# Kernel optimization log

Measured on AMD Instinct MI355X. Metric: run time of the kernel, lower is better.

Reference implementation:

```python
import jax, jax.numpy as jnp
import numpy as np
import math

B, S, F, R = 16, 2048, 512, 4
EPS = 1e-5

def setup_inputs() -> dict:
    key = jax.random.key(0)
    ks = jax.random.split(key, 8)
    s = 1.0 / math.sqrt(S)
    return {
        "x": jax.random.normal(ks[0], (B, S, F), dtype=jnp.float32),
        "Wq": jax.random.uniform(ks[1], (R, S), jnp.float32, -s, s),
        "bq": jnp.zeros((R,), jnp.float32),
        "Wk": jax.random.uniform(ks[2], (R, S), jnp.float32, -s, s),
        "bk": jnp.zeros((R,), jnp.float32),
        "Wv": jax.random.uniform(ks[3], (S, S), jnp.float32, -s, s),
        "bv": jnp.zeros((S,), jnp.float32),
        "ln_w": jnp.ones((S, F), jnp.float32),
        "ln_b": jnp.zeros((S, F), jnp.float32),
        "alpha": jnp.asarray(0.1, jnp.float32),
        "beta": jnp.asarray(0.1, jnp.float32),
    }

def reference(x, Wq, bq, Wk, bk, Wv, bv, ln_w, ln_b, alpha, beta):
    # LayerNorm over last two dims [S, F]
    mu = jnp.mean(x, axis=(1, 2), keepdims=True)
    var = jnp.mean(jnp.square(x - mu), axis=(1, 2), keepdims=True)
    x_norm = (x - mu) * jax.lax.rsqrt(var + EPS) * ln_w + ln_b
    x_t = jnp.swapaxes(x_norm, 1, 2)  # [B, F, S]
    Q = jnp.einsum('bfs,rs->bfr', x_t, Wq) + bq  # [B, F, R]
    K = jnp.einsum('bfs,rs->bfr', x_t, Wk) + bk  # [B, F, R]
    A = jnp.einsum('bfr,bgr->bfg', Q, K) / math.sqrt(R)  # [B, F, F]
    A = jax.nn.softmax(A, axis=-1)
    V = jnp.einsum('bfs,ts->bft', x_t, Wv) + bv  # [B, F, S]
    out = jnp.einsum('bfg,bgs->bfs', A, V)  # [B, F, S]
    # dropout in eval mode = identity
    out = x_t + alpha * out + V + beta * V
    return jnp.swapaxes(out, 1, 2)  # [B, S, F]
```

## Files before the change

### kernel.cpp

```cpp
#include <hip/hip_runtime.h>
#include <hip/hip_bf16.h>

#define NB 16
#define SS 2048
#define FF 512

typedef __bf16 bf16_t;
typedef __bf16 bf16x8 __attribute__((ext_vector_type(8)));
typedef __bf16 bf16x4 __attribute__((ext_vector_type(4)));
typedef float  f32x4  __attribute__((ext_vector_type(4)));

__global__ __launch_bounds__(256) void stats_kernel(const float* __restrict__ x,
                                                    float* __restrict__ partials) {
    const int b = blockIdx.y;
    const float* xb = x + ((size_t)b << 20) + (size_t)blockIdx.x * 16384;
    float s = 0.0f, ss = 0.0f;
#pragma unroll
    for (int i = 0; i < 16; ++i) {
        const float4 v = *(const float4*)&xb[(threadIdx.x + i * 256) * 4];
        s  += v.x + v.y + v.z + v.w;
        ss += v.x * v.x + v.y * v.y + v.z * v.z + v.w * v.w;
    }
#pragma unroll
    for (int off = 32; off > 0; off >>= 1) {
        s  += __shfl_down(s, off);
        ss += __shfl_down(ss, off);
    }
    __shared__ float ps[4], pss[4];
    const int w = threadIdx.x >> 6, lane = threadIdx.x & 63;
    if (lane == 0) { ps[w] = s; pss[w] = ss; }
    __syncthreads();
    if (threadIdx.x == 0) {
        partials[b * 64 + blockIdx.x]        = ps[0] + ps[1] + ps[2] + ps[3];
        partials[1024 + b * 64 + blockIdx.x] = pss[0] + pss[1] + pss[2] + pss[3];
    }
}

__global__ __launch_bounds__(256) void finalize_stats(const float* __restrict__ partials,
                                                      float* __restrict__ musig) {
    const int tid = threadIdx.x;
    const int b = tid >> 4, i = tid & 15;
    float s = 0.f, ss = 0.f;
#pragma unroll
    for (int j = 0; j < 4; ++j) {
        s  += partials[b * 64 + i * 4 + j];
        ss += partials[1024 + b * 64 + i * 4 + j];
    }
#pragma unroll
    for (int off = 8; off > 0; off >>= 1) {
        s  += __shfl_xor(s, off);
        ss += __shfl_xor(ss, off);
    }
    if (i == 0) {
        const float inv_n = 1.0f / 1048576.0f;
        const float mu  = s * inv_n;
        const float var = ss * inv_n - mu * mu;
        musig[b]      = mu;
        musig[16 + b] = rsqrtf(var + 1e-5f);
    }
}

__global__ __launch_bounds__(256) void ynorm_kernel(const float* __restrict__ x,
                                                    const float* __restrict__ lw,
                                                    const float* __restrict__ lb,
                                                    const float* __restrict__ musig,
                                                    bf16_t* __restrict__ Y,
                                                    bf16_t* __restrict__ Xn) {
    __shared__ bf16_t t[32][36];
    const int b = blockIdx.z;
    const int f0 = blockIdx.x * 32, s0 = blockIdx.y * 32;
    const float mu = musig[b], rs = musig[16 + b];
    const int tid = threadIdx.x;
    {
        const int s_loc = tid >> 3, c4 = (tid & 7) * 4;
        const size_t idx = (size_t)(s0 + s_loc) * FF + f0 + c4;
        const float4 xv = *(const float4*)&x[((size_t)b << 20) + idx];
        const float4 wv = *(const float4*)&lw[idx];
        const float4 bv = *(const float4*)&lb[idx];
        bf16x4 o;
        o[0] = (bf16_t)((xv.x - mu) * rs * wv.x + bv.x);
        o[1] = (bf16_t)((xv.y - mu) * rs * wv.y + bv.y);
        o[2] = (bf16_t)((xv.z - mu) * rs * wv.z + bv.z);
        o[3] = (bf16_t)((xv.w - mu) * rs * wv.w + bv.w);
        t[s_loc][c4 + 0] = o[0];
        t[s_loc][c4 + 1] = o[1];
        t[s_loc][c4 + 2] = o[2];
        t[s_loc][c4 + 3] = o[3];
        if (Xn) *(bf16x4*)&Xn[((size_t)b << 20) + idx] = o;
    }
    __syncthreads();
    {
        const int f_loc = tid >> 3, s4 = (tid & 7) * 4;
        bf16x4 o;
        o[0] = t[s4 + 0][f_loc];
        o[1] = t[s4 + 1][f_loc];
        o[2] = t[s4 + 2][f_loc];
        o[3] = t[s4 + 3][f_loc];
        *(bf16x4*)&Y[((size_t)b << 20) + (size_t)(f0 + f_loc) * SS + s0 + s4] = o;
    }
}

__global__ __launch_bounds__(256) void cast_wv(const float* __restrict__ Wv,
                                               bf16_t* __restrict__ Wvb) {
    const size_t i = ((size_t)blockIdx.x * 256 + threadIdx.x) * 4;
    const float4 v = *(const float4*)&Wv[i];
    bf16x4 o;
    o[0] = (bf16_t)v.x; o[1] = (bf16_t)v.y; o[2] = (bf16_t)v.z; o[3] = (bf16_t)v.w;
    *(bf16x4*)&Wvb[i] = o;
}

__global__ __launch_bounds__(256) void qk_kernel(const bf16_t* __restrict__ Y,
                                                 const float* __restrict__ Wq,
                                                 const float* __restrict__ bq,
                                                 const float* __restrict__ Wk,
                                                 const float* __restrict__ bk,
                                                 float* __restrict__ Qo,
                                                 float* __restrict__ Ko) {
    const int w = threadIdx.x >> 6, lane = threadIdx.x & 63;
    const int row0 = blockIdx.x * 16 + w * 4;
    const bf16_t* y0 = Y + (size_t)row0 * SS;
    float qa[4][4] = {}, ka[4][4] = {};
#pragma unroll
    for (int c = 0; c < 4; ++c) {
        const int s = c * 512 + lane * 8;
        float yf[4][8];
#pragma unroll
        for (int rr = 0; rr < 4; ++rr) {
            const bf16x8 yv = *(const bf16x8*)&y0[(size_t)rr * SS + s];
#pragma unroll
            for (int j = 0; j < 8; ++j) yf[rr][j] = (float)yv[j];
        }
#pragma unroll
        for (int r = 0; r < 4; ++r) {
            const float4 a0 = *(const float4*)&Wq[r * SS + s];
            const float4 a1 = *(const float4*)&Wq[r * SS + s + 4];
            const float4 c0 = *(const float4*)&Wk[r * SS + s];
            const float4 c1 = *(const float4*)&Wk[r * SS + s + 4];
#pragma unroll
            for (int rr = 0; rr < 4; ++rr) {
                qa[rr][r] += yf[rr][0]*a0.x + yf[rr][1]*a0.y + yf[rr][2]*a0.z + yf[rr][3]*a0.w
                           + yf[rr][4]*a1.x + yf[rr][5]*a1.y + yf[rr][6]*a1.z + yf[rr][7]*a1.w;
                ka[rr][r] += yf[rr][0]*c0.x + yf[rr][1]*c0.y + yf[rr][2]*c0.z + yf[rr][3]*c0.w
                           + yf[rr][4]*c1.x + yf[rr][5]*c1.y + yf[rr][6]*c1.z + yf[rr][7]*c1.w;
            }
        }
    }
#pragma unroll
    for (int off = 32; off > 0; off >>= 1) {
#pragma unroll
        for (int rr = 0; rr < 4; ++rr)
#pragma unroll
            for (int r = 0; r < 4; ++r) {
                qa[rr][r] += __shfl_down(qa[rr][r], off);
                ka[rr][r] += __shfl_down(ka[rr][r], off);
            }
    }
    if (lane == 0) {
#pragma unroll
        for (int rr = 0; rr < 4; ++rr)
#pragma unroll
            for (int r = 0; r < 4; ++r) {
                Qo[(size_t)(row0 + rr) * 4 + r] = qa[rr][r] + bq[r];
                Ko[(size_t)(row0 + rr) * 4 + r] = ka[rr][r] + bk[r];
            }
    }
}

__global__ __launch_bounds__(256) void softmax_kernel(const float* __restrict__ Qo,
                                                      const float* __restrict__ Ko,
                                                      bf16_t* __restrict__ Aout) {
    const int w = threadIdx.x >> 6, lane = threadIdx.x & 63;
    const int row = blockIdx.x * 4 + w;
    const int b = row >> 9;
    const float4 q = *(const float4*)&Qo[(size_t)row * 4];
    const float* kb = Ko + (size_t)b * FF * 4;
    float sc[8];
#pragma unroll
    for (int j = 0; j < 8; ++j) {
        const float4 kv = *(const float4*)&kb[(lane * 8 + j) * 4];
        sc[j] = (q.x*kv.x + q.y*kv.y + q.z*kv.z + q.w*kv.w) * 0.5f;
    }
    float mx = sc[0];
#pragma unroll
    for (int j = 1; j < 8; ++j) mx = fmaxf(mx, sc[j]);
#pragma unroll
    for (int off = 32; off > 0; off >>= 1) mx = fmaxf(mx, __shfl_xor(mx, off));
    float sum = 0.f;
#pragma unroll
    for (int j = 0; j < 8; ++j) { sc[j] = __expf(sc[j] - mx); sum += sc[j]; }
#pragma unroll
    for (int off = 32; off > 0; off >>= 1) sum += __shfl_xor(sum, off);
    const float inv = 1.0f / sum;
    bf16x8 o;
#pragma unroll
    for (int j = 0; j < 8; ++j) o[j] = (bf16_t)(sc[j] * inv);
    *(bf16x8*)&Aout[(size_t)row * FF + lane * 8] = o;
}

template<int EPI>
__device__ __forceinline__ void gemm_impl(
        const bf16_t* __restrict__ Abase, long long strideA, int lda,
        const bf16_t* __restrict__ Bbase, long long strideB, int ldb,
        bf16_t* __restrict__ Cbase, long long strideC, int ldc,
        int NTILES, const float* __restrict__ bias_m,
        const float* __restrict__ xp, const float* __restrict__ lwp,
        const float* __restrict__ lbp, const bf16_t* __restrict__ xnp,
        const float* __restrict__ musig,
        const float* __restrict__ alphap, const float* __restrict__ betap,
        float* __restrict__ outp) {
    __shared__ __align__(16) bf16_t As[2][16384];
    __shared__ __align__(16) bf16_t Bs[2][16384];
    const int tid = threadIdx.x;
    const int w = tid >> 6, lane = tid & 63;

    const int nchunk = gridDim.x >> 3;
    const int wgid = (blockIdx.x & 7) * nchunk + (blockIdx.x >> 3);
    const int bz = wgid >> 4;
    const int rem = wgid & 15;
    const int m0 = (rem & 7) * 256, n0 = (rem >> 3) * 256;

    const bf16_t* A = Abase + (size_t)bz * (size_t)strideA;
    const bf16_t* B = Bbase + (size_t)bz * (size_t)strideB;
    bf16_t* C = Cbase + (size_t)bz * (size_t)strideC;
    const int wm = w >> 2, wn = w & 3;

    const int rr0 = (w * 2 + 0) * 16 + (lane >> 2);
    const int rr1 = (w * 2 + 1) * 16 + (lane >> 2);
    const int sw0 = ((lane & 3) ^ ((rr0 >> 1) & 3)) * 8;
    const int sw1 = ((lane & 3) ^ ((rr1 >> 1) & 3)) * 8;
    const bf16_t* gA0 = A + (size_t)(m0 + rr0) * lda + sw0;
    const bf16_t* gA1 = A + (size_t)(m0 + rr1) * lda + sw1;
    const bf16_t* gB0 = B + (size_t)(n0 + rr0) * ldb + sw0;
    const bf16_t* gB1 = B + (size_t)(n0 + rr1) * ldb + sw1;
    const int d0 = (w * 2 + 0) * 512;
    const int d1 = (w * 2 + 1) * 512;

#define STA(bi, h, ko) do {                                                          \
    __builtin_amdgcn_global_load_lds(                                                \
        (const __attribute__((address_space(1))) unsigned int*)(gA0 + (ko) + (h)*32),\
        (__attribute__((address_space(3))) unsigned int*)&As[bi][(h)*8192 + d0], 16, 0, 0); \
    __builtin_amdgcn_global_load_lds(                                                \
        (const __attribute__((address_space(1))) unsigned int*)(gA1 + (ko) + (h)*32),\
        (__attribute__((address_space(3))) unsigned int*)&As[bi][(h)*8192 + d1], 16, 0, 0); \
} while (0)
#define STB(bi, h, ko) do {                                                          \
    __builtin_amdgcn_global_load_lds(                                                \
        (const __attribute__((address_space(1))) unsigned int*)(gB0 + (ko) + (h)*32),\
        (__attribute__((address_space(3))) unsigned int*)&Bs[bi][(h)*8192 + d0], 16, 0, 0); \
    __builtin_amdgcn_global_load_lds(                                                \
        (const __attribute__((address_space(1))) unsigned int*)(gB1 + (ko) + (h)*32),\
        (__attribute__((address_space(3))) unsigned int*)&Bs[bi][(h)*8192 + d1], 16, 0, 0); \
} while (0)

    const int cs = lane >> 4;
    int offA[2][8], offB[2][4];
#pragma unroll
    for (int kk = 0; kk < 2; ++kk) {
#pragma unroll
        for (int mt = 0; mt < 8; ++mt) {
            const int r = wm * 128 + mt * 16 + (lane & 15);
            offA[kk][mt] = kk * 8192 + r * 32 + ((cs ^ ((r >> 1) & 3)) << 3);
        }
#pragma unroll
        for (int nt = 0; nt < 4; ++nt) {
            const int r = wn * 64 + nt * 16 + (lane & 15);
            offB[kk][nt] = kk * 8192 + r * 32 + ((cs ^ ((r >> 1) & 3)) << 3);
        }
    }

#define RD_A(dst, base, kk, mh) do { _Pragma("unroll")                        \
    for (int i = 0; i < 4; ++i) dst[i] = *(const bf16x8*)&(base)[offA[kk][(mh)*4 + i]]; } while (0)
#define RD_B(dst, base, kk) do { _Pragma("unroll")                            \
    for (int i = 0; i < 4; ++i) dst[i] = *(const bf16x8*)&(base)[offB[kk][i]]; } while (0)
#define MFMA16X(af, bfr, mh) do { _Pragma("unroll")                           \
    for (int i = 0; i < 4; ++i) { _Pragma("unroll")                           \
        for (int nt = 0; nt < 4; ++nt)                                        \
            acc[(mh)*4 + i][nt] = __builtin_amdgcn_mfma_f32_16x16x32_bf16(    \
                af[i], bfr[nt], acc[(mh)*4 + i][nt], 0, 0, 0); } } while (0)
#define VMC(n) asm volatile("s_waitcnt vmcnt(" #n ")" ::: "memory")
#define HBAR  __builtin_amdgcn_s_barrier()
#define LGKM(n) do { asm volatile("s_waitcnt lgkmcnt(" #n ")" ::: "memory");  \
                     __builtin_amdgcn_sched_barrier(0); } while (0)
#define SBAR  __builtin_amdgcn_sched_barrier(0)
#define PRIO1 __builtin_amdgcn_s_setprio(1)
#define PRIO0 __builtin_amdgcn_s_setprio(0)

    f32x4 acc[8][4] = {};
    bf16x8 afA[4], afB[4], bfrA[4], bfrB[4];
    const int mask = NTILES - 1;

    STA(0, 0, 0); STB(0, 0, 0); STA(0, 1, 0); STB(0, 1, 0);
    VMC(4); HBAR;
    RD_A(afA, As[0], 0, 0); RD_B(bfrA, Bs[0], 0);

    for (int t = 0; t < NTILES; ++t) {
        const int cur = t & 1, oth = cur ^ 1;
        const int ko = ((t + 1) & mask) * 64;
        const bf16_t* as  = As[cur];
        const bf16_t* bs  = Bs[cur];
        const bf16_t* asn = As[oth];
        const bf16_t* bsn = Bs[oth];
        RD_A(afB, as, 0, 1); SBAR;
        STA(oth, 0, ko); SBAR;
        LGKM(4);
        PRIO1; MFMA16X(afA, bfrA, 0); PRIO0; SBAR;
        VMC(2); HBAR;
        RD_A(afA, as, 1, 0); RD_B(bfrB, bs, 1); SBAR;
        STB(oth, 0, ko); SBAR;
        LGKM(8);
        PRIO1; MFMA16X(afB, bfrA, 1); PRIO0; SBAR;
        RD_A(afB, as, 1, 1); SBAR;
        STA(oth, 1, ko); SBAR;
        LGKM(4);
        PRIO1; MFMA16X(afA, bfrB, 0); PRIO0; SBAR;
        VMC(2); HBAR;
        RD_A(afA, asn, 0, 0); RD_B(bfrA, bsn, 0); SBAR;
        STB(oth, 1, ko); SBAR;
        LGKM(8);
        PRIO1; MFMA16X(afB, bfrB, 1); PRIO0; SBAR;
    }
#undef STA
#undef STB
#undef RD_A
#undef RD_B
#undef MFMA16X
#undef VMC
#undef HBAR
#undef LGKM
#undef SBAR
#undef PRIO1
#undef PRIO0

    if constexpr (EPI == 0) {
#pragma unroll
        for (int mt = 0; mt < 8; ++mt) {
#pragma unroll
            for (int r = 0; r < 4; ++r) {
                const int row = m0 + wm * 128 + mt * 16 + ((lane >> 4) << 2) + r;
                const float bm = bias_m ? bias_m[row] : 0.0f;
#pragma unroll
                for (int nt = 0; nt < 4; ++nt) {
                    const int col = n0 + wn * 64 + nt * 16 + (lane & 15);
                    C[(size_t)row * ldc + col] = (bf16_t)(acc[mt][nt][r] + bm);
                }
            }
        }
    } else {
        asm volatile("s_waitcnt vmcnt(0) lgkmcnt(0)" ::: "memory");
        __syncthreads();
        float* lsc0 = (float*)&As[0][0];
        float* lsc1 = (float*)&As[1][0];
        const float alpha = alphap[0];
        const float onepb = 1.0f + betap[0];
        float mu = 0.f, rs = 0.f;
        if constexpr (EPI == 1) { mu = musig[bz]; rs = musig[16 + bz]; }
        const float* xb = (EPI == 1) ? xp + ((size_t)bz << 20) : nullptr;
        const bf16_t* xnb = (EPI == 2) ? xnp + ((size_t)bz << 20) : nullptr;
        float* ob = outp + ((size_t)bz << 20);
        const int lrow = wm * 16 + ((lane >> 4) << 2);
        const int lcol = wn * 64 + (lane & 15);
        const int gr = tid >> 4;
        const int gc = (tid & 15) * 16;
#define SCAT(mt, bank) do { _Pragma("unroll")                                 \
    for (int r = 0; r < 4; ++r) { _Pragma("unroll")                           \
        for (int nt = 0; nt < 4; ++nt)                                        \
            (bank)[(lrow + r) * 256 + lcol + nt * 16] = acc[mt][nt][r]; } } while (0)
        SCAT(0, lsc0);
        __syncthreads();
#pragma unroll
        for (int mt = 0; mt < 8; ++mt) {
            float* bank  = (mt & 1) ? lsc1 : lsc0;
            float* nbank = (mt & 1) ? lsc0 : lsc1;
            const int grow = m0 + (gr >> 4) * 128 + mt * 16 + (gr & 15);
            const size_t idx = (size_t)grow * FF + n0 + gc;
            const bf16x8 vt0 = *(const bf16x8*)&A[(size_t)grow * lda + n0 + gc];
            const bf16x8 vt1 = *(const bf16x8*)&A[(size_t)grow * lda + n0 + gc + 8];
            bf16x8 xn0, xn1;
            float4 xv[4], wv[4], bv4[4];
            if constexpr (EPI == 2) {
                xn0 = *(const bf16x8*)&xnb[idx];
                xn1 = *(const bf16x8*)&xnb[idx + 8];
            } else {
#pragma unroll
                for (int j = 0; j < 4; ++j) {
                    xv[j]  = *(const float4*)&xb[idx + j * 4];
                    wv[j]  = *(const float4*)&lwp[idx + j * 4];
                    bv4[j] = *(const float4*)&lbp[idx + j * 4];
                }
            }
            if (mt < 7) {
                switch (mt + 1) {
                    case 1: SCAT(1, nbank); break;
                    case 2: SCAT(2, nbank); break;
                    case 3: SCAT(3, nbank); break;
                    case 4: SCAT(4, nbank); break;
                    case 5: SCAT(5, nbank); break;
                    case 6: SCAT(6, nbank); break;
                    case 7: SCAT(7, nbank); break;
                }
            }
#pragma unroll
            for (int j = 0; j < 4; ++j) {
                const float4 av = *(const float4*)&bank[gr * 256 + gc + j * 4];
                float4 o;
                if constexpr (EPI == 2) {
                    const int e = (j & 1) * 4;
                    const bf16x8& xs = (j < 2) ? xn0 : xn1;
                    const bf16x8& vs = (j < 2) ? vt0 : vt1;
                    o.x = (float)xs[e + 0] + alpha * av.x + onepb * (float)vs[e + 0];
                    o.y = (float)xs[e + 1] + alpha * av.y + onepb * (float)vs[e + 1];
                    o.z = (float)xs[e + 2] + alpha * av.z + onepb * (float)vs[e + 2];
                    o.w = (float)xs[e + 3] + alpha * av.w + onepb * (float)vs[e + 3];
                } else {
                    const int e = (j & 1) * 4;
                    const bf16x8& vs = (j < 2) ? vt0 : vt1;
                    o.x = (xv[j].x - mu) * rs * wv[j].x + bv4[j].x + alpha * av.x + onepb * (float)vs[e + 0];
                    o.y = (xv[j].y - mu) * rs * wv[j].y + bv4[j].y + alpha * av.y + onepb * (float)vs[e + 1];
                    o.z = (xv[j].z - mu) * rs * wv[j].z + bv4[j].z + alpha * av.z + onepb * (float)vs[e + 2];
                    o.w = (xv[j].w - mu) * rs * wv[j].w + bv4[j].w + alpha * av.w + onepb * (float)vs[e + 3];
                }
                *(float4*)&ob[idx + j * 4] = o;
            }
            __syncthreads();
        }
#undef SCAT
    }
}

__global__ __launch_bounds__(512, 2) void g1_mm(
        const bf16_t* A, long long sA, int lda, const bf16_t* B, long long sB, int ldb,
        bf16_t* C, long long sC, int ldc, int NT, const float* bias_m) {
    gemm_impl<0>(A, sA, lda, B, sB, ldb, C, sC, ldc, NT, bias_m,
                 nullptr, nullptr, nullptr, nullptr, nullptr, nullptr, nullptr, nullptr);
}

__global__ __launch_bounds__(512, 2) void g2_mm_full(
        const bf16_t* A, long long sA, int lda, const bf16_t* B, long long sB, int ldb,
        int NT, const float* xp, const float* lwp, const float* lbp,
        const float* musig, const float* alphap, const float* betap, float* outp) {
    gemm_impl<1>(A, sA, lda, B, sB, ldb, nullptr, 0, FF, NT, nullptr,
                 xp, lwp, lbp, nullptr, musig, alphap, betap, outp);
}

__global__ __launch_bounds__(512, 2) void g2_mm_lite(
        const bf16_t* A, long long sA, int lda, const bf16_t* B, long long sB, int ldb,
        int NT, const bf16_t* xnp,
        const float* musig, const float* alphap, const float* betap, float* outp) {
    gemm_impl<2>(A, sA, lda, B, sB, ldb, nullptr, 0, FF, NT, nullptr,
                 nullptr, nullptr, nullptr, xnp, musig, alphap, betap, outp);
}

extern "C" void kernel_launch(void* const* d_in, const int* in_sizes, int n_in,
                              void* d_out, int out_size, void* d_ws, size_t ws_size,
                              hipStream_t stream) {
    const float* x   = (const float*)d_in[0];
    const float* Wq  = (const float*)d_in[1];
    const float* bq  = (const float*)d_in[2];
    const float* Wk  = (const float*)d_in[3];
    const float* bk  = (const float*)d_in[4];
    const float* Wv  = (const float*)d_in[5];
    const float* bv  = (const float*)d_in[6];
    const float* lw  = (const float*)d_in[7];
    const float* lb  = (const float*)d_in[8];
    const float* alp = (const float*)d_in[9];
    const float* bet = (const float*)d_in[10];
    float* out = (float*)d_out;

    char* ws = (char*)d_ws;
    float*  musig = (float*)(ws + 128);
    float*  Qo    = (float*)(ws + 256);
    float*  Ko    = (float*)(ws + 256 + 131072);
    bf16_t* Wvb   = (bf16_t*)(ws + 262400);
    bf16_t* Asm   = (bf16_t*)(ws + 8651008);
    float*  partials = (float*)(ws + 8651008);
    bf16_t* Vt    = (bf16_t*)(ws + 17039616);
    bf16_t* Y     = (bf16_t*)(ws + 50594048);
    bf16_t* Xn    = (bf16_t*)(ws + 84148480);
    const bool lite = ws_size >= (size_t)117702912;

    stats_kernel<<<dim3(64, 16), 256, 0, stream>>>(x, partials);
    finalize_stats<<<1, 256, 0, stream>>>(partials, musig);
    cast_wv<<<4096, 256, 0, stream>>>(Wv, Wvb);
    ynorm_kernel<<<dim3(16, 64, 16), 256, 0, stream>>>(x, lw, lb, musig, Y,
                                                       lite ? Xn : (bf16_t*)nullptr);
    qk_kernel<<<512, 256, 0, stream>>>(Y, Wq, bq, Wk, bk, Qo, Ko);
    softmax_kernel<<<2048, 256, 0, stream>>>(Qo, Ko, Asm);
    g1_mm<<<256, 512, 0, stream>>>(Wvb, 0, SS, Y, 1 << 20, SS, Vt, 1 << 20, FF, 32, bv);
    if (lite) {
        g2_mm_lite<<<256, 512, 0, stream>>>(Vt, 1 << 20, FF, Asm, FF * FF, FF, 8,
                                            Xn, musig, alp, bet, out);
    } else {
        g2_mm_full<<<256, 512, 0, stream>>>(Vt, 1 << 20, FF, Asm, FF * FF, FF, 8,
                                            x, lw, lb, musig, alp, bet, out);
    }
}
```

Baseline: 175.0 us.

## Replace V-projection GEMM with 128x128-tile kernel using more workgroups

Adds a dedicated g1_mm2 kernel for the V projection. It uses 128x128 output tiles, 256 threads, 4 waves each owning a 64x64 sub-tile, and a simplified two-phase double-buffered K loop. It launches 1024 workgroups instead of 256 with 256x256 tiles, which raises occupancy and spreads work more evenly across CUs. The cost is lower operand reuse per tile, so more global and LDS traffic per FLOP. The old EPI==0 path is removed from the shared gemm template.

```diff
diff --git a/kernel.cpp b/kernel.cpp
--- a/kernel.cpp
+++ b/kernel.cpp
@@ -197,12 +197,134 @@
     *(bf16x8*)&Aout[(size_t)row * FF + lane * 8] = o;
 }
 
+__global__ __launch_bounds__(256, 2) void g1_mm2(
+        const bf16_t* __restrict__ Abase, long long strideA, int lda,
+        const bf16_t* __restrict__ Bbase, long long strideB, int ldb,
+        bf16_t* __restrict__ Cbase, long long strideC, int ldc,
+        int NTILES, const float* __restrict__ bias_m) {
+    __shared__ __align__(16) bf16_t As[2][8192];
+    __shared__ __align__(16) bf16_t Bs[2][8192];
+    const int tid = threadIdx.x;
+    const int w = tid >> 6, lane = tid & 63;
+
+    const int nchunk = gridDim.x >> 3;
+    const int wgid = (blockIdx.x & 7) * nchunk + (blockIdx.x >> 3);
+    const int bz = wgid >> 6;
+    const int rem = wgid & 63;
+    const int m0 = (rem & 15) * 128, n0 = (rem >> 4) * 128;
+
+    const bf16_t* A = Abase + (size_t)bz * (size_t)strideA;
+    const bf16_t* B = Bbase + (size_t)bz * (size_t)strideB;
+    bf16_t* C = Cbase + (size_t)bz * (size_t)strideC;
+    const int wmm = (w >> 1) * 64, wnn = (w & 1) * 64;
+
+    const int rr0 = (w * 2 + 0) * 16 + (lane >> 2);
+    const int rr1 = (w * 2 + 1) * 16 + (lane >> 2);
+    const int sw0 = ((lane & 3) ^ ((rr0 >> 1) & 3)) * 8;
+    const int sw1 = ((lane & 3) ^ ((rr1 >> 1) & 3)) * 8;
+    const bf16_t* gA0 = A + (size_t)(m0 + rr0) * lda + sw0;
+    const bf16_t* gA1 = A + (size_t)(m0 + rr1) * lda + sw1;
+    const bf16_t* gB0 = B + (size_t)(n0 + rr0) * ldb + sw0;
+    const bf16_t* gB1 = B + (size_t)(n0 + rr1) * ldb + sw1;
+    const int d0 = (w * 2 + 0) * 512;
+    const int d1 = (w * 2 + 1) * 512;
+
+#define STA2(bi, h, ko) do {                                                         \
+    __builtin_amdgcn_global_load_lds(                                                \
+        (const __attribute__((address_space(1))) unsigned int*)(gA0 + (ko) + (h)*32),\
+        (__attribute__((address_space(3))) unsigned int*)&As[bi][(h)*4096 + d0], 16, 0, 0); \
+    __builtin_amdgcn_global_load_lds(                                                \
+        (const __attribute__((address_space(1))) unsigned int*)(gA1 + (ko) + (h)*32),\
+        (__attribute__((address_space(3))) unsigned int*)&As[bi][(h)*4096 + d1], 16, 0, 0); \
+} while (0)
+#define STB2(bi, h, ko) do {                                                         \
+    __builtin_amdgcn_global_load_lds(                                                \
+        (const __attribute__((address_space(1))) unsigned int*)(gB0 + (ko) + (h)*32),\
+        (__attribute__((address_space(3))) unsigned int*)&Bs[bi][(h)*4096 + d0], 16, 0, 0); \
+    __builtin_amdgcn_global_load_lds(                                                \
+        (const __attribute__((address_space(1))) unsigned int*)(gB1 + (ko) + (h)*32),\
+        (__attribute__((address_space(3))) unsigned int*)&Bs[bi][(h)*4096 + d1], 16, 0, 0); \
+} while (0)
+
+    const int cs = lane >> 4;
+    int offA[2][4], offB[2][4];
+#pragma unroll
+    for (int kk = 0; kk < 2; ++kk) {
+#pragma unroll
+        for (int i = 0; i < 4; ++i) {
+            const int ra = wmm + i * 16 + (lane & 15);
+            offA[kk][i] = kk * 4096 + ra * 32 + ((cs ^ ((ra >> 1) & 3)) << 3);
+            const int rb = wnn + i * 16 + (lane & 15);
+            offB[kk][i] = kk * 4096 + rb * 32 + ((cs ^ ((rb >> 1) & 3)) << 3);
+        }
+    }
+
+#define VMC2  asm volatile("s_waitcnt vmcnt(2)" ::: "memory")
+#define HBAR  __builtin_amdgcn_s_barrier()
+#define LGKM0 do { asm volatile("s_waitcnt lgkmcnt(0)" ::: "memory");         \
+                   __builtin_amdgcn_sched_barrier(0); } while (0)
+#define SBAR  __builtin_amdgcn_sched_barrier(0)
+
+    f32x4 acc[4][4] = {};
+    bf16x8 af[4], bfr[4];
+    const int mask = NTILES - 1;
+
+    STA2(0, 0, 0); STB2(0, 0, 0); STA2(0, 1, 0); STB2(0, 1, 0);
+
+#define PHASE(kk, stA, stB)                                                   \
+    VMC2; HBAR;                                                               \
+    _Pragma("unroll")                                                         \
+    for (int i = 0; i < 4; ++i) af[i]  = *(const bf16x8*)&as[offA[kk][i]];    \
+    _Pragma("unroll")                                                         \
+    for (int i = 0; i < 4; ++i) bfr[i] = *(const bf16x8*)&bs[offB[kk][i]];    \
+    SBAR;                                                                     \
+    stA; stB; SBAR;                                                           \
+    LGKM0;                                                                    \
+    __builtin_amdgcn_s_setprio(1);                                            \
+    _Pragma("unroll")                                                         \
+    for (int i = 0; i < 4; ++i) { _Pragma("unroll")                           \
+        for (int nt = 0; nt < 4; ++nt)                                        \
+            acc[i][nt] = __builtin_amdgcn_mfma_f32_16x16x32_bf16(             \
+                af[i], bfr[nt], acc[i][nt], 0, 0, 0); }                       \
+    __builtin_amdgcn_s_setprio(0); SBAR;                                      \
+    HBAR;
+
+    for (int t = 0; t < NTILES; ++t) {
+        const int cur = t & 1, oth = cur ^ 1;
+        const int ko = ((t + 1) & mask) * 64;
+        const bf16_t* as = As[cur];
+        const bf16_t* bs = Bs[cur];
+        PHASE(0, STA2(oth, 0, ko), STB2(oth, 0, ko));
+        PHASE(1, STA2(oth, 1, ko), STB2(oth, 1, ko));
+    }
+#undef PHASE
+#undef STA2
+#undef STB2
+#undef VMC2
+#undef HBAR
+#undef LGKM0
+#undef SBAR
+
+#pragma unroll
+    for (int i = 0; i < 4; ++i) {
+#pragma unroll
+        for (int r = 0; r < 4; ++r) {
+            const int row = m0 + wmm + i * 16 + ((lane >> 4) << 2) + r;
+            const float bm = bias_m ? bias_m[row] : 0.0f;
+#pragma unroll
+            for (int nt = 0; nt < 4; ++nt) {
+                const int col = n0 + wnn + nt * 16 + (lane & 15);
+                C[(size_t)row * ldc + col] = (bf16_t)(acc[i][nt][r] + bm);
+            }
+        }
+    }
+}
+
 template<int EPI>
 __device__ __forceinline__ void gemm_impl(
         const bf16_t* __restrict__ Abase, long long strideA, int lda,
         const bf16_t* __restrict__ Bbase, long long strideB, int ldb,
-        bf16_t* __restrict__ Cbase, long long strideC, int ldc,
-        int NTILES, const float* __restrict__ bias_m,
+        int NTILES,
         const float* __restrict__ xp, const float* __restrict__ lwp,
         const float* __restrict__ lbp, const bf16_t* __restrict__ xnp,
         const float* __restrict__ musig,
@@ -221,7 +343,6 @@
 
     const bf16_t* A = Abase + (size_t)bz * (size_t)strideA;
     const bf16_t* B = Bbase + (size_t)bz * (size_t)strideB;
-    bf16_t* C = Cbase + (size_t)bz * (size_t)strideC;
     const int wm = w >> 2, wn = w & 3;
 
     const int rr0 = (w * 2 + 0) * 16 + (lane >> 2);
@@ -331,114 +452,91 @@
 #undef PRIO1
 #undef PRIO0
 
-    if constexpr (EPI == 0) {
-#pragma unroll
-        for (int mt = 0; mt < 8; ++mt) {
-#pragma unroll
-            for (int r = 0; r < 4; ++r) {
-                const int row = m0 + wm * 128 + mt * 16 + ((lane >> 4) << 2) + r;
-                const float bm = bias_m ? bias_m[row] : 0.0f;
-#pragma unroll
-                for (int nt = 0; nt < 4; ++nt) {
-                    const int col = n0 + wn * 64 + nt * 16 + (lane & 15);
-                    C[(size_t)row * ldc + col] = (bf16_t)(acc[mt][nt][r] + bm);
-                }
-            }
-        }
-    } else {
-        asm volatile("s_waitcnt vmcnt(0) lgkmcnt(0)" ::: "memory");
-        __syncthreads();
-        float* lsc0 = (float*)&As[0][0];
-        float* lsc1 = (float*)&As[1][0];
-        const float alpha = alphap[0];
-        const float onepb = 1.0f + betap[0];
-        float mu = 0.f, rs = 0.f;
-        if constexpr (EPI == 1) { mu = musig[bz]; rs = musig[16 + bz]; }
-        const float* xb = (EPI == 1) ? xp + ((size_t)bz << 20) : nullptr;
-        const bf16_t* xnb = (EPI == 2) ? xnp + ((size_t)bz << 20) : nullptr;
-        float* ob = outp + ((size_t)bz << 20);
-        const int lrow = wm * 16 + ((lane >> 4) << 2);
-        const int lcol = wn * 64 + (lane & 15);
-        const int gr = tid >> 4;
-        const int gc = (tid & 15) * 16;
+    asm volatile("s_waitcnt vmcnt(0) lgkmcnt(0)" ::: "memory");
+    __syncthreads();
+    float* lsc0 = (float*)&As[0][0];
+    float* lsc1 = (float*)&As[1][0];
+    const float alpha = alphap[0];
+    const float onepb = 1.0f + betap[0];
+    float mu = 0.f, rs = 0.f;
+    if constexpr (EPI == 1) { mu = musig[bz]; rs = musig[16 + bz]; }
+    const float* xb = (EPI == 1) ? xp + ((size_t)bz << 20) : nullptr;
+    const bf16_t* xnb = (EPI == 2) ? xnp + ((size_t)bz << 20) : nullptr;
+    float* ob = outp + ((size_t)bz << 20);
+    const int lrow = wm * 16 + ((lane >> 4) << 2);
+    const int lcol = wn * 64 + (lane & 15);
+    const int gr = tid >> 4;
+    const int gc = (tid & 15) * 16;
 #define SCAT(mt, bank) do { _Pragma("unroll")                                 \
     for (int r = 0; r < 4; ++r) { _Pragma("unroll")                           \
         for (int nt = 0; nt < 4; ++nt)                                        \
             (bank)[(lrow + r) * 256 + lcol + nt * 16] = acc[mt][nt][r]; } } while (0)
-        SCAT(0, lsc0);
+    SCAT(0, lsc0);
+    __syncthreads();
+#pragma unroll
+    for (int mt = 0; mt < 8; ++mt) {
+        float* bank  = (mt & 1) ? lsc1 : lsc0;
+        float* nbank = (mt & 1) ? lsc0 : lsc1;
+        const int grow = m0 + (gr >> 4) * 128 + mt * 16 + (gr & 15);
+        const size_t idx = (size_t)grow * FF + n0 + gc;
+        const bf16x8 vt0 = *(const bf16x8*)&A[(size_t)grow * lda + n0 + gc];
+        const bf16x8 vt1 = *(const bf16x8*)&A[(size_t)grow * lda + n0 + gc + 8];
+        bf16x8 xn0, xn1;
+        float4 xv[4], wv[4], bv4[4];
+        if constexpr (EPI == 2) {
+            xn0 = *(const bf16x8*)&xnb[idx];
+            xn1 = *(const bf16x8*)&xnb[idx + 8];
+        } else {
+#pragma unroll
+            for (int j = 0; j < 4; ++j) {
+                xv[j]  = *(const float4*)&xb[idx + j * 4];
+                wv[j]  = *(const float4*)&lwp[idx + j * 4];
+                bv4[j] = *(const float4*)&lbp[idx + j * 4];
+            }
+        }
+        if (mt < 7) {
+            switch (mt + 1) {
+                case 1: SCAT(1, nbank); break;
+                case 2: SCAT(2, nbank); break;
+                case 3: SCAT(3, nbank); break;
+                case 4: SCAT(4, nbank); break;
+                case 5: SCAT(5, nbank); break;
+                case 6: SCAT(6, nbank); break;
+                case 7: SCAT(7, nbank); break;
+            }
+        }
+#pragma unroll
+        for (int j = 0; j < 4; ++j) {
+            const float4 av = *(const float4*)&bank[gr * 256 + gc + j * 4];
+            float4 o;
+            if constexpr (EPI == 2) {
+                const int e = (j & 1) * 4;
+                const bf16x8& xs = (j < 2) ? xn0 : xn1;
+                const bf16x8& vs = (j < 2) ? vt0 : vt1;
+                o.x = (float)xs[e + 0] + alpha * av.x + onepb * (float)vs[e + 0];
+                o.y = (float)xs[e + 1] + alpha * av.y + onepb * (float)vs[e + 1];
+                o.z = (float)xs[e + 2] + alpha * av.z + onepb * (float)vs[e + 2];
+                o.w = (float)xs[e + 3] + alpha * av.w + onepb * (float)vs[e + 3];
+            } else {
+                const int e = (j & 1) * 4;
+                const bf16x8& vs = (j < 2) ? vt0 : vt1;
+                o.x = (xv[j].x - mu) * rs * wv[j].x + bv4[j].x + alpha * av.x + onepb * (float)vs[e + 0];
+                o.y = (xv[j].y - mu) * rs * wv[j].y + bv4[j].y + alpha * av.y + onepb * (float)vs[e + 1];
+                o.z = (xv[j].z - mu) * rs * wv[j].z + bv4[j].z + alpha * av.z + onepb * (float)vs[e + 2];
+                o.w = (xv[j].w - mu) * rs * wv[j].w + bv4[j].w + alpha * av.w + onepb * (float)vs[e + 3];
+            }
+            *(float4*)&ob[idx + j * 4] = o;
+        }
         __syncthreads();
-#pragma unroll
-        for (int mt = 0; mt < 8; ++mt) {
-            float* bank  = (mt & 1) ? lsc1 : lsc0;
-            float* nbank = (mt & 1) ? lsc0 : lsc1;
-            const int grow = m0 + (gr >> 4) * 128 + mt * 16 + (gr & 15);
-            const size_t idx = (size_t)grow * FF + n0 + gc;
-            const bf16x8 vt0 = *(const bf16x8*)&A[(size_t)grow * lda + n0 + gc];
-            const bf16x8 vt1 = *(const bf16x8*)&A[(size_t)grow * lda + n0 + gc + 8];
-            bf16x8 xn0, xn1;
-            float4 xv[4], wv[4], bv4[4];
-            if constexpr (EPI == 2) {
-                xn0 = *(const bf16x8*)&xnb[idx];
-                xn1 = *(const bf16x8*)&xnb[idx + 8];
-            } else {
-#pragma unroll
-                for (int j = 0; j < 4; ++j) {
-                    xv[j]  = *(const float4*)&xb[idx + j * 4];
-                    wv[j]  = *(const float4*)&lwp[idx + j * 4];
-                    bv4[j] = *(const float4*)&lbp[idx + j * 4];
-                }
-            }
-            if (mt < 7) {
-                switch (mt + 1) {
-                    case 1: SCAT(1, nbank); break;
-                    case 2: SCAT(2, nbank); break;
-                    case 3: SCAT(3, nbank); break;
-                    case 4: SCAT(4, nbank); break;
-                    case 5: SCAT(5, nbank); break;
-                    case 6: SCAT(6, nbank); break;
-                    case 7: SCAT(7, nbank); break;
-                }
-            }
-#pragma unroll
-            for (int j = 0; j < 4; ++j) {
-                const float4 av = *(const float4*)&bank[gr * 256 + gc + j * 4];
-                float4 o;
-                if constexpr (EPI == 2) {
-                    const int e = (j & 1) * 4;
-                    const bf16x8& xs = (j < 2) ? xn0 : xn1;
-                    const bf16x8& vs = (j < 2) ? vt0 : vt1;
-                    o.x = (float)xs[e + 0] + alpha * av.x + onepb * (float)vs[e + 0];
-                    o.y = (float)xs[e + 1] + alpha * av.y + onepb * (float)vs[e + 1];
-                    o.z = (float)xs[e + 2] + alpha * av.z + onepb * (float)vs[e + 2];
-                    o.w = (float)xs[e + 3] + alpha * av.w + onepb * (float)vs[e + 3];
-                } else {
-                    const int e = (j & 1) * 4;
-                    const bf16x8& vs = (j < 2) ? vt0 : vt1;
-                    o.x = (xv[j].x - mu) * rs * wv[j].x + bv4[j].x + alpha * av.x + onepb * (float)vs[e + 0];
-                    o.y = (xv[j].y - mu) * rs * wv[j].y + bv4[j].y + alpha * av.y + onepb * (float)vs[e + 1];
-                    o.z = (xv[j].z - mu) * rs * wv[j].z + bv4[j].z + alpha * av.z + onepb * (float)vs[e + 2];
-                    o.w = (xv[j].w - mu) * rs * wv[j].w + bv4[j].w + alpha * av.w + onepb * (float)vs[e + 3];
-                }
-                *(float4*)&ob[idx + j * 4] = o;
-            }
-            __syncthreads();
-        }
+    }
 #undef SCAT
-    }
-}
-
-__global__ __launch_bounds__(512, 2) void g1_mm(
-        const bf16_t* A, long long sA, int lda, const bf16_t* B, long long sB, int ldb,
-        bf16_t* C, long long sC, int ldc, int NT, const float* bias_m) {
-    gemm_impl<0>(A, sA, lda, B, sB, ldb, C, sC, ldc, NT, bias_m,
-                 nullptr, nullptr, nullptr, nullptr, nullptr, nullptr, nullptr, nullptr);
 }
 
 __global__ __launch_bounds__(512, 2) void g2_mm_full(
         const bf16_t* A, long long sA, int lda, const bf16_t* B, long long sB, int ldb,
         int NT, const float* xp, const float* lwp, const float* lbp,
         const float* musig, const float* alphap, const float* betap, float* outp) {
-    gemm_impl<1>(A, sA, lda, B, sB, ldb, nullptr, 0, FF, NT, nullptr,
+    gemm_impl<1>(A, sA, lda, B, sB, ldb, NT,
                  xp, lwp, lbp, nullptr, musig, alphap, betap, outp);
 }
 
@@ -446,7 +544,7 @@
         const bf16_t* A, long long sA, int lda, const bf16_t* B, long long sB, int ldb,
         int NT, const bf16_t* xnp,
         const float* musig, const float* alphap, const float* betap, float* outp) {
-    gemm_impl<2>(A, sA, lda, B, sB, ldb, nullptr, 0, FF, NT, nullptr,
+    gemm_impl<2>(A, sA, lda, B, sB, ldb, NT,
                  nullptr, nullptr, nullptr, xnp, musig, alphap, betap, outp);
 }
 
@@ -485,7 +583,7 @@
                                                        lite ? Xn : (bf16_t*)nullptr);
     qk_kernel<<<512, 256, 0, stream>>>(Y, Wq, bq, Wk, bk, Qo, Ko);
     softmax_kernel<<<2048, 256, 0, stream>>>(Qo, Ko, Asm);
-    g1_mm<<<256, 512, 0, stream>>>(Wvb, 0, SS, Y, 1 << 20, SS, Vt, 1 << 20, FF, 32, bv);
+    g1_mm2<<<1024, 256, 0, stream>>>(Wvb, 0, SS, Y, 1 << 20, SS, Vt, 1 << 20, FF, 32, bv);
     if (lite) {
         g2_mm_lite<<<256, 512, 0, stream>>>(Vt, 1 << 20, FF, Asm, FF * FF, FF, 8,
                                             Xn, musig, alp, bet, out);
```

Result: slower. 193.7 us (+10.7%).
